# Performance work log

Measured on AMD Instinct MI355X. Metric: run time of the kernel, lower is better.

Reference implementation:

```python
import jax, jax.numpy as jnp
import numpy as np

B, S = 4, 1024
IN_F, OUT_F = 8192, 8192
ACT_BITS = 8


def setup_inputs() -> dict:
    key = jax.random.key(0)
    k1, k2, k3, k4 = jax.random.split(key, 4)
    x = jax.random.normal(k1, (B, S, IN_F), dtype=jnp.float32)
    # each int8 byte packs two 4-bit exponent nibbles; stored as int32 values in [0, 256)
    packed_exponents = jax.random.randint(k2, (OUT_F, IN_F // 2), 0, 256, dtype=jnp.int32)
    # signs are +/-1 per weight element
    signs = jax.random.randint(k3, (OUT_F, IN_F), 0, 2, dtype=jnp.int32) * 2 - 1
    bias = jax.random.normal(k4, (OUT_F,), dtype=jnp.float32)
    activation_scale = jnp.float32(0.02)  # delta_lsb for int8 activation quant
    min_exp = -14  # python int constant (buffer min_exp in the torch module)
    return {
        "x": x,
        "packed_exponents": packed_exponents,
        "signs": signs,
        "bias": bias,
        "activation_scale": activation_scale,
        "min_exp": min_exp,
    }


def reference(x, packed_exponents, signs, bias, activation_scale, min_exp):
    q_max = 2 ** (ACT_BITS - 1) - 1   # 127
    q_min = -2 ** (ACT_BITS - 1)      # -128
    orig_shape = x.shape
    x2 = x.reshape(-1, orig_shape[-1])  # [N, IN_F]

    # int8 activation quantization (kept in float; values are exact small ints)
    a_quant = jnp.clip(jnp.round(x2 / activation_scale), q_min, q_max)

    # unpack two 4-bit exponent nibbles per byte: low nibble first, then high
    lo = packed_exponents & 0xF
    hi = (packed_exponents >> 4) & 0xF
    exps = jnp.stack([lo, hi], axis=-1).reshape(OUT_F, IN_F)  # [OUT_F, IN_F]

    # dequantized log-domain weights: sign * 2^(nibble + min_exp)
    w = signs.astype(jnp.float32) * jnp.exp2((exps + min_exp).astype(jnp.float32))

    # batched matvec (the CUDA kernel does one row of this per launch) + dequant + bias
    out = (a_quant @ w.T) * activation_scale + bias  # [N, OUT_F]
    return out.reshape(*orig_shape[:-1], OUT_F)
```

## Files before the change

kernel.cpp:

```cpp
#include <hip/hip_runtime.h>
#include <hip/hip_bf16.h>
#include <stdint.h>

#define N_TOK 4096
#define KF    8192
#define NF    8192

#define BM 256
#define BN 256

typedef __attribute__((ext_vector_type(8))) short short8;
typedef __attribute__((ext_vector_type(4))) float f32x4;

#define GLOBAL_P(p) ((const __attribute__((address_space(1))) void*)(p))
#define LDS_P(p)    ((__attribute__((address_space(3))) void*)(p))

__global__ void quant_x(const float* __restrict__ x, const float* __restrict__ scale_p,
                        uint16_t* __restrict__ a) {
    const float s = *scale_p;
    const int n8 = N_TOK * KF / 8;
    const int stride = gridDim.x * blockDim.x;
    for (int i = blockIdx.x * blockDim.x + threadIdx.x; i < n8; i += stride) {
        const float4* xp = (const float4*)(x + (size_t)i * 8);
        float4 v0 = xp[0], v1 = xp[1];
        float q[8] = {v0.x, v0.y, v0.z, v0.w, v1.x, v1.y, v1.z, v1.w};
        union { uint16_t u16[8]; short8 v; } o;
        #pragma unroll
        for (int j = 0; j < 8; ++j) {
            float t = rintf(q[j] / s);
            t = fminf(fmaxf(t, -128.f), 127.f);
            union { float f; uint32_t u; } cv; cv.f = t;
            o.u16[j] = (uint16_t)(cv.u >> 16);
        }
        *(short8*)(a + (size_t)i * 8) = o.v;
    }
}

__global__ void dequant_w(const int* __restrict__ packed, const int* __restrict__ signs,
                          const int* __restrict__ minexp_p, uint16_t* __restrict__ w) {
    const int me = *minexp_p;
    const int ebase = (me + 127) << 7;
    const int n4 = NF * (KF / 2) / 4;
    const int stride = gridDim.x * blockDim.x;
    for (int i = blockIdx.x * blockDim.x + threadIdx.x; i < n4; i += stride) {
        int4 p  = ((const int4*)packed)[i];
        int4 s0 = ((const int4*)signs)[(size_t)i * 2];
        int4 s1 = ((const int4*)signs)[(size_t)i * 2 + 1];
        int pw[4] = {p.x, p.y, p.z, p.w};
        int sg[8] = {s0.x, s0.y, s0.z, s0.w, s1.x, s1.y, s1.z, s1.w};
        union { uint16_t u16[8]; short8 v; } o;
        #pragma unroll
        for (int j = 0; j < 4; ++j) {
            int lo = pw[j] & 0xF, hi = (pw[j] >> 4) & 0xF;
            o.u16[2 * j]     = (uint16_t)((ebase + (lo << 7)) | (sg[2 * j]     < 0 ? 0x8000 : 0));
            o.u16[2 * j + 1] = (uint16_t)((ebase + (hi << 7)) | (sg[2 * j + 1] < 0 ? 0x8000 : 0));
        }
        *(short8*)(w + (size_t)i * 8) = o.v;
    }
}

#define BARRIER()  __builtin_amdgcn_s_barrier()
#define SCHED0()   __builtin_amdgcn_sched_barrier(0)
#define WAITVM4()  do { asm volatile("s_waitcnt vmcnt(4)"); SCHED0(); } while (0)
#define WAITVM0()  do { asm volatile("s_waitcnt vmcnt(0)"); SCHED0(); } while (0)
#define SP1 __builtin_amdgcn_s_setprio(1)
#define SP0 __builtin_amdgcn_s_setprio(0)

__global__ __launch_bounds__(512, 2) void gemm_bt(
        const uint16_t* __restrict__ A, const uint16_t* __restrict__ W,
        const float* __restrict__ bias, const float* __restrict__ scale_p,
        float* __restrict__ out) {
    __shared__ uint16_t ldsA[4 * 256 * 32];
    __shared__ uint16_t ldsB[4 * 256 * 32];

    const int tid  = threadIdx.x;
    const int wid  = tid >> 6, lane = tid & 63;
    const int wr = wid >> 2, wc = wid & 3;
    const int rlane = lane & 15, kgrp = lane >> 4;

    const int bid = blockIdx.x;
    const int xcd = bid & 7;
    const int i_l = bid >> 3;
    const int gen = i_l >> 5;
    const int il  = i_l & 31;
    const int by  = gen * 8 + (il >> 2);
    const int bx  = xcd * 4 + (il & 3);
    const int rowA0 = by * BM;
    const int colB0 = bx * BN;

    const int o0 = tid * 16, o1 = (512 + tid) * 16;
    const int l0 = o0 ^ (((o0 >> 9) & 1) << 5);
    const int l1 = o1 ^ (((o1 >> 9) & 1) << 5);
    const char* gA0 = (const char*)A + ((size_t)(rowA0 + (l0 >> 6)) * KF) * 2 + (l0 & 63);
    const char* gA1 = (const char*)A + ((size_t)(rowA0 + (l1 >> 6)) * KF) * 2 + (l1 & 63);
    const char* gB0 = (const char*)W + ((size_t)(colB0 + (l0 >> 6)) * KF) * 2 + (l0 & 63);
    const char* gB1 = (const char*)W + ((size_t)(colB0 + (l1 >> 6)) * KF) * 2 + (l1 & 63);
    const int ldst0 = wid * 1024;
    const int ldst1 = 8192 + wid * 1024;

    int aoff[8], boff[4];
    #pragma unroll
    for (int i = 0; i < 8; ++i) {
        int row = wr * 128 + i * 16 + rlane;
        int o = row * 64 + kgrp * 16;
        aoff[i] = o ^ (((o >> 9) & 1) << 5);
    }
    #pragma unroll
    for (int n = 0; n < 4; ++n) {
        int row = wc * 64 + n * 16 + rlane;
        int o = row * 64 + kgrp * 16;
        boff[n] = o ^ (((o >> 9) & 1) << 5);
    }

#define STAGE_A(j) do { \
    char* b_ = (char*)ldsA + ((j) & 3) * 16384; \
    __builtin_amdgcn_global_load_lds(GLOBAL_P(gA0 + (size_t)(j) * 64), LDS_P(b_ + ldst0), 16, 0, 0); \
    __builtin_amdgcn_global_load_lds(GLOBAL_P(gA1 + (size_t)(j) * 64), LDS_P(b_ + ldst1), 16, 0, 0); \
} while (0)
#define STAGE_B(j) do { \
    char* b_ = (char*)ldsB + ((j) & 3) * 16384; \
    __builtin_amdgcn_global_load_lds(GLOBAL_P(gB0 + (size_t)(j) * 64), LDS_P(b_ + ldst0), 16, 0, 0); \
    __builtin_amdgcn_global_load_lds(GLOBAL_P(gB1 + (size_t)(j) * 64), LDS_P(b_ + ldst1), 16, 0, 0); \
} while (0)
#define LDAH(DST, H, SLOT) do { \
    const char* p_ = (const char*)ldsA + (SLOT) * 16384; \
    _Pragma("unroll") for (int i_ = 0; i_ < 4; ++i_) \
        DST[i_] = *(const short8*)(p_ + aoff[(H) * 4 + i_]); \
} while (0)
#define LDB4(DST, SLOT) do { \
    const char* p_ = (const char*)ldsB + (SLOT) * 16384; \
    _Pragma("unroll") for (int i_ = 0; i_ < 4; ++i_) \
        DST[i_] = *(const short8*)(p_ + boff[i_]); \
} while (0)
#define MFMAH(H, A4, B4) do { \
    SP1; \
    _Pragma("unroll") for (int mm_ = 0; mm_ < 4; ++mm_) \
        _Pragma("unroll") for (int nn_ = 0; nn_ < 4; ++nn_) \
            acc[(H) * 4 + mm_][nn_] = __builtin_amdgcn_mfma_f32_16x16x32_bf16( \
                A4[mm_], B4[nn_], acc[(H) * 4 + mm_][nn_], 0, 0, 0); \
    SP0; \
} while (0)

#define WINDOW(BC, BN_, SC, SN, JST, VM) do { \
    BARRIER(); \
    LDAH(aQ, 1, SC);             \
    STAGE_A(JST); \
    MFMAH(0, aP, BC); \
    LDAH(aP, 0, SN);             \
    LDB4(BN_, SN);               \
    STAGE_B(JST); \
    MFMAH(1, aQ, BC); \
    VM; \
} while (0)
#define WINDOW_NS(BC, BN_, SC, SN, VM) do { \
    BARRIER(); \
    LDAH(aQ, 1, SC); \
    MFMAH(0, aP, BC); \
    LDAH(aP, 0, SN); \
    LDB4(BN_, SN); \
    MFMAH(1, aQ, BC); \
    VM; \
} while (0)

    f32x4 acc[8][4] = {};
    short8 aP[4], aQ[4], bP[4], bQ[4];

    STAGE_A(0); STAGE_B(0);
    STAGE_A(1); STAGE_B(1);
    STAGE_A(2); STAGE_B(2);
    WAITVM4();
    BARRIER();
    LDAH(aP, 0, 0);
    LDB4(bP, 0);

    for (int kt = 0; kt < 63; ++kt) {
        const int j0 = 4 * kt;
        WINDOW(bP, bQ, 0, 1, j0 + 3, WAITVM4());
        WINDOW(bQ, bP, 1, 2, j0 + 4, WAITVM4());
        WINDOW(bP, bQ, 2, 3, j0 + 5, WAITVM4());
        WINDOW(bQ, bP, 3, 0, j0 + 6, WAITVM4());
    }

    WINDOW(bP, bQ, 0, 1, 255, WAITVM4());
    WINDOW_NS(bQ, bP, 1, 2, WAITVM0());
    WINDOW_NS(bP, bQ, 2, 3, (void)0);
    BARRIER();
    LDAH(aQ, 1, 3);
    MFMAH(0, aP, bQ);
    MFMAH(1, aQ, bQ);

    const float s = *scale_p;
    const int colbase = colB0 + wc * 64 + rlane;
    const int rowbase = rowA0 + wr * 128 + kgrp * 4;
    #pragma unroll
    for (int n = 0; n < 4; ++n) {
        const float bv = bias[colbase + n * 16];
        #pragma unroll
        for (int mf = 0; mf < 8; ++mf) {
            #pragma unroll
            for (int r = 0; r < 4; ++r)
                out[(size_t)(rowbase + mf * 16 + r) * NF + colbase + n * 16] = acc[mf][n][r] * s + bv;
        }
    }
#undef STAGE_A
#undef STAGE_B
#undef LDAH
#undef LDB4
#undef MFMAH
#undef WINDOW
#undef WINDOW_NS
}

extern "C" void kernel_launch(void* const* d_in, const int* in_sizes, int n_in,
                              void* d_out, int out_size, void* d_ws, size_t ws_size,
                              hipStream_t stream) {
    const float* x      = (const float*)d_in[0];
    const int*   packed = (const int*)d_in[1];
    const int*   signs  = (const int*)d_in[2];
    const float* bias   = (const float*)d_in[3];
    const float* scale  = (const float*)d_in[4];
    const int*   minexp = (const int*)d_in[5];
    float* out = (float*)d_out;

    uint16_t* A = (uint16_t*)d_ws;
    uint16_t* W = (uint16_t*)((char*)d_ws + (size_t)N_TOK * KF * 2);

    quant_x<<<2048, 256, 0, stream>>>(x, scale, A);
    dequant_w<<<2048, 256, 0, stream>>>(packed, signs, minexp, W);
    gemm_bt<<<(N_TOK / BM) * (NF / BN), 512, 0, stream>>>(A, W, bias, scale, out);
}
```

Measured before the change: 604.2 us.

## Switch GEMM inner loop to 32x32x16 bf16 MFMA with new LDS swizzle

Replaces the 16x16x32 bf16 MFMA tiling (8x4 fragments per wave) with 32x32x16 MFMAs (4x2 fragments), splitting each 32-wide K slice into two K=16 steps. The LDS swizzle changes to a 2-bit XOR over 16-byte chunks, matching the new fragment read pattern, and the epilogue is rewritten for the 32x32 accumulator layout. The aim is fewer MFMA issues and LDS fragment reads per K step, since B fragments now cover 32 columns. In exchange, each instruction has longer latency, the register allocation for accumulators changes, and the epilogue stores follow a different pattern.

```diff
diff --git a/kernel.cpp b/kernel.cpp
--- a/kernel.cpp
+++ b/kernel.cpp
@@ -10,7 +10,7 @@
 #define BN 256
 
 typedef __attribute__((ext_vector_type(8))) short short8;
-typedef __attribute__((ext_vector_type(4))) float f32x4;
+typedef __attribute__((ext_vector_type(16))) float f32x16;
 
 #define GLOBAL_P(p) ((const __attribute__((address_space(1))) void*)(p))
 #define LDS_P(p)    ((__attribute__((address_space(3))) void*)(p))
@@ -66,6 +66,8 @@
 #define SP1 __builtin_amdgcn_s_setprio(1)
 #define SP0 __builtin_amdgcn_s_setprio(0)
 
+#define SWZ(o) ((o) ^ ((((o) >> 7) & 3) << 4))
+
 __global__ __launch_bounds__(512, 2) void gemm_bt(
         const uint16_t* __restrict__ A, const uint16_t* __restrict__ W,
         const float* __restrict__ bias, const float* __restrict__ scale_p,
@@ -76,7 +78,7 @@
     const int tid  = threadIdx.x;
     const int wid  = tid >> 6, lane = tid & 63;
     const int wr = wid >> 2, wc = wid & 3;
-    const int rlane = lane & 15, kgrp = lane >> 4;
+    const int rlane = lane & 31, khalf = lane >> 5;
 
     const int bid = blockIdx.x;
     const int xcd = bid & 7;
@@ -89,8 +91,8 @@
     const int colB0 = bx * BN;
 
     const int o0 = tid * 16, o1 = (512 + tid) * 16;
-    const int l0 = o0 ^ (((o0 >> 9) & 1) << 5);
-    const int l1 = o1 ^ (((o1 >> 9) & 1) << 5);
+    const int l0 = SWZ(o0);
+    const int l1 = SWZ(o1);
     const char* gA0 = (const char*)A + ((size_t)(rowA0 + (l0 >> 6)) * KF) * 2 + (l0 & 63);
     const char* gA1 = (const char*)A + ((size_t)(rowA0 + (l1 >> 6)) * KF) * 2 + (l1 & 63);
     const char* gB0 = (const char*)W + ((size_t)(colB0 + (l0 >> 6)) * KF) * 2 + (l0 & 63);
@@ -100,16 +102,18 @@
 
     int aoff[8], boff[4];
     #pragma unroll
-    for (int i = 0; i < 8; ++i) {
-        int row = wr * 128 + i * 16 + rlane;
-        int o = row * 64 + kgrp * 16;
-        aoff[i] = o ^ (((o >> 9) & 1) << 5);
-    }
-    #pragma unroll
-    for (int n = 0; n < 4; ++n) {
-        int row = wc * 64 + n * 16 + rlane;
-        int o = row * 64 + kgrp * 16;
-        boff[n] = o ^ (((o >> 9) & 1) << 5);
+    for (int ks = 0; ks < 2; ++ks) {
+        const int cb = ks * 32 + khalf * 16;
+        #pragma unroll
+        for (int m = 0; m < 4; ++m) {
+            int o = (wr * 128 + m * 32 + rlane) * 64 + cb;
+            aoff[ks * 4 + m] = SWZ(o);
+        }
+        #pragma unroll
+        for (int n = 0; n < 2; ++n) {
+            int o = (wc * 64 + n * 32 + rlane) * 64 + cb;
+            boff[ks * 2 + n] = SWZ(o);
+        }
     }
 
 #define STAGE_A(j) do { \
@@ -122,91 +126,91 @@
     __builtin_amdgcn_global_load_lds(GLOBAL_P(gB0 + (size_t)(j) * 64), LDS_P(b_ + ldst0), 16, 0, 0); \
     __builtin_amdgcn_global_load_lds(GLOBAL_P(gB1 + (size_t)(j) * 64), LDS_P(b_ + ldst1), 16, 0, 0); \
 } while (0)
-#define LDAH(DST, H, SLOT) do { \
+#define LDA_K(DST, KS, SLOT) do { \
     const char* p_ = (const char*)ldsA + (SLOT) * 16384; \
     _Pragma("unroll") for (int i_ = 0; i_ < 4; ++i_) \
-        DST[i_] = *(const short8*)(p_ + aoff[(H) * 4 + i_]); \
-} while (0)
-#define LDB4(DST, SLOT) do { \
+        DST[i_] = *(const short8*)(p_ + aoff[(KS) * 4 + i_]); \
+} while (0)
+#define LDB_K(DST, KS, SLOT) do { \
     const char* p_ = (const char*)ldsB + (SLOT) * 16384; \
-    _Pragma("unroll") for (int i_ = 0; i_ < 4; ++i_) \
-        DST[i_] = *(const short8*)(p_ + boff[i_]); \
-} while (0)
-#define MFMAH(H, A4, B4) do { \
+    _Pragma("unroll") for (int i_ = 0; i_ < 2; ++i_) \
+        DST[i_] = *(const short8*)(p_ + boff[(KS) * 2 + i_]); \
+} while (0)
+#define MFMA8(A4, B2) do { \
     SP1; \
     _Pragma("unroll") for (int mm_ = 0; mm_ < 4; ++mm_) \
-        _Pragma("unroll") for (int nn_ = 0; nn_ < 4; ++nn_) \
-            acc[(H) * 4 + mm_][nn_] = __builtin_amdgcn_mfma_f32_16x16x32_bf16( \
-                A4[mm_], B4[nn_], acc[(H) * 4 + mm_][nn_], 0, 0, 0); \
+        _Pragma("unroll") for (int nn_ = 0; nn_ < 2; ++nn_) \
+            acc[mm_][nn_] = __builtin_amdgcn_mfma_f32_32x32x16_bf16( \
+                A4[mm_], B2[nn_], acc[mm_][nn_], 0, 0, 0); \
     SP0; \
 } while (0)
 
-#define WINDOW(BC, BN_, SC, SN, JST, VM) do { \
+#define WINDOW(SC, SN, JST, VM) do { \
     BARRIER(); \
-    LDAH(aQ, 1, SC);             \
+    LDA_K(aQ, 1, SC); LDB_K(bQ, 1, SC); \
     STAGE_A(JST); \
-    MFMAH(0, aP, BC); \
-    LDAH(aP, 0, SN);             \
-    LDB4(BN_, SN);               \
+    MFMA8(aP, bP); \
+    LDA_K(aP, 0, SN); LDB_K(bP, 0, SN); \
     STAGE_B(JST); \
-    MFMAH(1, aQ, BC); \
+    MFMA8(aQ, bQ); \
     VM; \
 } while (0)
-#define WINDOW_NS(BC, BN_, SC, SN, VM) do { \
+#define WINDOW_NS(SC, SN, VM) do { \
     BARRIER(); \
-    LDAH(aQ, 1, SC); \
-    MFMAH(0, aP, BC); \
-    LDAH(aP, 0, SN); \
-    LDB4(BN_, SN); \
-    MFMAH(1, aQ, BC); \
+    LDA_K(aQ, 1, SC); LDB_K(bQ, 1, SC); \
+    MFMA8(aP, bP); \
+    LDA_K(aP, 0, SN); LDB_K(bP, 0, SN); \
+    MFMA8(aQ, bQ); \
     VM; \
 } while (0)
 
-    f32x4 acc[8][4] = {};
-    short8 aP[4], aQ[4], bP[4], bQ[4];
+    f32x16 acc[4][2] = {};
+    short8 aP[4], aQ[4], bP[2], bQ[2];
 
     STAGE_A(0); STAGE_B(0);
     STAGE_A(1); STAGE_B(1);
     STAGE_A(2); STAGE_B(2);
     WAITVM4();
     BARRIER();
-    LDAH(aP, 0, 0);
-    LDB4(bP, 0);
+    LDA_K(aP, 0, 0);
+    LDB_K(bP, 0, 0);
 
     for (int kt = 0; kt < 63; ++kt) {
         const int j0 = 4 * kt;
-        WINDOW(bP, bQ, 0, 1, j0 + 3, WAITVM4());
-        WINDOW(bQ, bP, 1, 2, j0 + 4, WAITVM4());
-        WINDOW(bP, bQ, 2, 3, j0 + 5, WAITVM4());
-        WINDOW(bQ, bP, 3, 0, j0 + 6, WAITVM4());
-    }
-
-    WINDOW(bP, bQ, 0, 1, 255, WAITVM4());
-    WINDOW_NS(bQ, bP, 1, 2, WAITVM0());
-    WINDOW_NS(bP, bQ, 2, 3, (void)0);
+        WINDOW(0, 1, j0 + 3, WAITVM4());
+        WINDOW(1, 2, j0 + 4, WAITVM4());
+        WINDOW(2, 3, j0 + 5, WAITVM4());
+        WINDOW(3, 0, j0 + 6, WAITVM4());
+    }
+
+    WINDOW(0, 1, 255, WAITVM4());
+    WINDOW_NS(1, 2, WAITVM0());
+    WINDOW_NS(2, 3, (void)0);
     BARRIER();
-    LDAH(aQ, 1, 3);
-    MFMAH(0, aP, bQ);
-    MFMAH(1, aQ, bQ);
+    LDA_K(aQ, 1, 3); LDB_K(bQ, 1, 3);
+    MFMA8(aP, bP);
+    MFMA8(aQ, bQ);
 
     const float s = *scale_p;
     const int colbase = colB0 + wc * 64 + rlane;
-    const int rowbase = rowA0 + wr * 128 + kgrp * 4;
+    const int rowbase = rowA0 + wr * 128 + 4 * khalf;
     #pragma unroll
-    for (int n = 0; n < 4; ++n) {
-        const float bv = bias[colbase + n * 16];
-        #pragma unroll
-        for (int mf = 0; mf < 8; ++mf) {
+    for (int n = 0; n < 2; ++n) {
+        const float bv = bias[colbase + n * 32];
+        #pragma unroll
+        for (int mb = 0; mb < 4; ++mb) {
             #pragma unroll
-            for (int r = 0; r < 4; ++r)
-                out[(size_t)(rowbase + mf * 16 + r) * NF + colbase + n * 16] = acc[mf][n][r] * s + bv;
+            for (int r = 0; r < 16; ++r) {
+                const int row = rowbase + mb * 32 + (r & 3) + 8 * (r >> 2);
+                out[(size_t)row * NF + colbase + n * 32] = acc[mb][n][r] * s + bv;
+            }
         }
     }
 #undef STAGE_A
 #undef STAGE_B
-#undef LDAH
-#undef LDB4
-#undef MFMAH
+#undef LDA_K
+#undef LDB_K
+#undef MFMA8
 #undef WINDOW
 #undef WINDOW_NS
 }
```

Measured after the change: 620.9 us. +2.8%, slower.

## Restructure GEMM register pipeline to prefetch full A tile and load B in-window

Applied to the files above, without the earlier changes.

Reorganizes the LDS-to-register software pipeline of the bf16 MFMA GEMM. The whole next A fragment (8 short8) is double-buffered across windows, and the B fragment is loaded at the start of each window from the current slot. Both global-to-LDS stages are now issued together. The aim is to give the LDS reads more time to land before the MFMAs that consume them. In exchange it raises register pressure (16 A vectors live) and the first MFMA group now depends on B reads issued right after the barrier.

```diff
diff --git a/kernel.cpp b/kernel.cpp
--- a/kernel.cpp
+++ b/kernel.cpp
@@ -125,69 +125,65 @@
 #define LDAH(DST, H, SLOT) do { \
     const char* p_ = (const char*)ldsA + (SLOT) * 16384; \
     _Pragma("unroll") for (int i_ = 0; i_ < 4; ++i_) \
-        DST[i_] = *(const short8*)(p_ + aoff[(H) * 4 + i_]); \
+        DST[(H) * 4 + i_] = *(const short8*)(p_ + aoff[(H) * 4 + i_]); \
 } while (0)
 #define LDB4(DST, SLOT) do { \
     const char* p_ = (const char*)ldsB + (SLOT) * 16384; \
     _Pragma("unroll") for (int i_ = 0; i_ < 4; ++i_) \
         DST[i_] = *(const short8*)(p_ + boff[i_]); \
 } while (0)
-#define MFMAH(H, A4, B4) do { \
+#define MFMAH(H, ARR, B4) do { \
     SP1; \
     _Pragma("unroll") for (int mm_ = 0; mm_ < 4; ++mm_) \
         _Pragma("unroll") for (int nn_ = 0; nn_ < 4; ++nn_) \
             acc[(H) * 4 + mm_][nn_] = __builtin_amdgcn_mfma_f32_16x16x32_bf16( \
-                A4[mm_], B4[nn_], acc[(H) * 4 + mm_][nn_], 0, 0, 0); \
+                ARR[(H) * 4 + mm_], B4[nn_], acc[(H) * 4 + mm_][nn_], 0, 0, 0); \
     SP0; \
 } while (0)
 
-#define WINDOW(BC, BN_, SC, SN, JST, VM) do { \
+#define WINDOW(CUR, NXT, SC, SN, JST, VM) do { \
     BARRIER(); \
-    LDAH(aQ, 1, SC);             \
-    STAGE_A(JST); \
-    MFMAH(0, aP, BC); \
-    LDAH(aP, 0, SN);             \
-    LDB4(BN_, SN);               \
-    STAGE_B(JST); \
-    MFMAH(1, aQ, BC); \
+    LDB4(bf, SC); \
+    STAGE_A(JST); STAGE_B(JST); \
+    MFMAH(0, CUR, bf); \
+    LDAH(NXT, 0, SN); LDAH(NXT, 1, SN); \
+    MFMAH(1, CUR, bf); \
     VM; \
 } while (0)
-#define WINDOW_NS(BC, BN_, SC, SN, VM) do { \
+#define WINDOW_NS(CUR, NXT, SC, SN, VM) do { \
     BARRIER(); \
-    LDAH(aQ, 1, SC); \
-    MFMAH(0, aP, BC); \
-    LDAH(aP, 0, SN); \
-    LDB4(BN_, SN); \
-    MFMAH(1, aQ, BC); \
+    LDB4(bf, SC); \
+    MFMAH(0, CUR, bf); \
+    LDAH(NXT, 0, SN); LDAH(NXT, 1, SN); \
+    MFMAH(1, CUR, bf); \
     VM; \
 } while (0)
 
     f32x4 acc[8][4] = {};
-    short8 aP[4], aQ[4], bP[4], bQ[4];
+    short8 aX[8], aY[8], bf[4];
 
     STAGE_A(0); STAGE_B(0);
     STAGE_A(1); STAGE_B(1);
     STAGE_A(2); STAGE_B(2);
     WAITVM4();
     BARRIER();
-    LDAH(aP, 0, 0);
-    LDB4(bP, 0);
+    LDAH(aX, 0, 0); LDAH(aX, 1, 0);
 
     for (int kt = 0; kt < 63; ++kt) {
         const int j0 = 4 * kt;
-        WINDOW(bP, bQ, 0, 1, j0 + 3, WAITVM4());
-        WINDOW(bQ, bP, 1, 2, j0 + 4, WAITVM4());
-        WINDOW(bP, bQ, 2, 3, j0 + 5, WAITVM4());
-        WINDOW(bQ, bP, 3, 0, j0 + 6, WAITVM4());
-    }
-
-    WINDOW(bP, bQ, 0, 1, 255, WAITVM4());
-    WINDOW_NS(bQ, bP, 1, 2, WAITVM0());
-    WINDOW_NS(bP, bQ, 2, 3, (void)0);
+        WINDOW(aX, aY, 0, 1, j0 + 3, WAITVM4());
+        WINDOW(aY, aX, 1, 2, j0 + 4, WAITVM4());
+        WINDOW(aX, aY, 2, 3, j0 + 5, WAITVM4());
+        WINDOW(aY, aX, 3, 0, j0 + 6, WAITVM4());
+    }
+
+    WINDOW(aX, aY, 0, 1, 255, WAITVM4());
+    WINDOW_NS(aY, aX, 1, 2, WAITVM0());
+    WINDOW_NS(aX, aY, 2, 3, (void)0);
     BARRIER();
-    LDAH(aQ, 1, 3);
-    MFMAH(0, aP, bQ);
-    MFMAH(1, aQ, bQ);
+    LDB4(bf, 3);
+    MFMAH(0, aY, bf);
+    MFMAH(1, aY, bf);
 
     const float s = *scale_p;
     const int colbase = colB0 + wc * 64 + rlane;
```

After: 646.7 us. 7.0% more time.
